# Performance work log

Measured on AMD Instinct MI355X. Metric: run time of the kernel, lower is better.

Reference implementation:

```python
import jax, jax.numpy as jnp
import numpy as np

MERGE_R = 2048


def setup_inputs() -> dict:
    key = jax.random.key(0)
    k1, k2 = jax.random.split(key, 2)
    B, N, C = 4, 8192, 512
    x = jax.random.normal(k1, (B, N, C), jnp.float32)
    W = jax.random.normal(k2, (C // 4, C), jnp.float32) * 0.02  # Linear(dim, dim//4)
    b = jnp.zeros((C // 4,), jnp.float32)
    return {"x": x, "W": W, "b": b}


def reference(x, W, b):
    B, N, C = x.shape
    r = min(MERGE_R, N // 2)

    # metric projection; matching is done under no_grad in the original
    metric = jax.lax.stop_gradient(x @ W.T + b)
    metric = metric / jnp.linalg.norm(metric, axis=-1, keepdims=True)

    a = metric[:, 0::2]   # [B, N/2, C/4] evens
    bt = metric[:, 1::2]  # [B, N/2, C/4] odds
    scores = jnp.einsum('bad,bcd->bac', a, bt)  # [B, N/2, N/2]
    values = scores.max(axis=-1)                # [B, N/2] best score per even token
    node_indices = scores.argmax(axis=-1)       # [B, N/2] best odd partner per even
    _, top_b_indices = jax.lax.top_k(values, r) # [B, r]

    bidx = jnp.arange(B)[:, None]
    global_b = top_b_indices * 2 + 1                                  # [B, r] odd positions removed
    matched_a = jnp.take_along_axis(node_indices, top_b_indices, 1)   # [B, r]
    global_a = matched_a * 2                                          # [B, r] even positions merged into

    # boolean keep-mask: exactly r False per row (topk indices are distinct)
    mask = jnp.ones((B, N), bool).at[bidx, global_b].set(False)

    b_feat = jnp.take_along_axis(x, global_b[:, :, None], axis=1)     # [B, r, C]
    x_out = x.at[bidx, global_a].add(b_feat)                          # scatter-add merge
    counts = jnp.ones((B, N, 1), x.dtype).at[bidx, global_a].add(1.0)
    x_out = x_out / counts

    # compact kept rows: stable argsort of ~mask keeps original order of True entries
    kept = jnp.argsort(~mask, axis=1)[:, : N - r]                     # [B, N-r]
    x_final = jnp.take_along_axis(x_out, kept[:, :, None], axis=1)    # [B, N-r, C]

    # ownership / unmerge map
    new_idx = jnp.cumsum(mask.astype(jnp.int32), axis=1) - 1          # [B, N]
    ownership = jnp.where(mask, new_idx, 0)
    target_a_new = jnp.take_along_axis(new_idx, global_a, axis=1)
    ownership = ownership.at[bidx, global_b].set(target_a_new)
    return x_final, ownership
```

## Files before the change

### kernel.cpp

```cpp
#include <hip/hip_runtime.h>
#include <cstdint>
#include <cstddef>

#define BQ    4
#define NTOK  8192
#define CDIM  512
#define MDIM  128
#define NA    4096
#define RSEL  2048
#define NKEEP (NTOK - RSEL)
#define RESCUE_CAP 2048
#define GAP_DELTA 2e-4f
#define WIN_TAU   2e-4f
#define CSPL  8

typedef float f32x4 __attribute__((ext_vector_type(4)));
typedef short short8 __attribute__((ext_vector_type(8)));

static __device__ __forceinline__ unsigned short bf16rne(float f) {
  unsigned u = __float_as_uint(f);
  return (unsigned short)((u + 0x7FFFu + ((u >> 16) & 1)) >> 16);
}

__device__ __forceinline__ unsigned long long rank_select_4096(
    const unsigned long long* keysL, unsigned* histL,
    unsigned long long* candL, unsigned* scanL, unsigned* shw ,
    int rank, int t) {
  unsigned long long pval = 0ull, pmask = 0ull;
  int curRank = rank;
  for (int lvl = 0; lvl < 3; ++lvl) {
    const int shift = 52 - lvl * 12;
#pragma unroll
    for (int i = 0; i < 4; ++i) histL[t + i * 1024] = 0;
    __syncthreads();
#pragma unroll
    for (int i = 0; i < 4; ++i) {
      unsigned long long k = keysL[t + i * 1024];
      if ((k & pmask) == pval)
        atomicAdd(&histL[(unsigned)((k >> shift) & 0xFFFull)], 1u);
    }
    __syncthreads();
    unsigned s = histL[4 * t] + histL[4 * t + 1] + histL[4 * t + 2] + histL[4 * t + 3];
    scanL[t] = s;
    __syncthreads();
    for (int off = 1; off < 1024; off <<= 1) {
      unsigned v = (t >= off) ? scanL[t - off] : 0;
      __syncthreads();
      scanL[t] += v;
      __syncthreads();
    }
    const unsigned incl = scanL[t], excl = incl - s;
    if ((int)excl <= curRank && curRank < (int)incl) {
      int r = curRank - (int)excl;
      unsigned b = 4 * t;
#pragma unroll
      for (int q = 0; q < 4; ++q) {
        unsigned c = histL[4 * t + q];
        if (r < (int)c) { b = 4 * t + q; break; }
        r -= (int)c;
      }
      shw[0] = b; shw[1] = (unsigned)r; shw[3] = histL[b];
    }
    __syncthreads();
    const unsigned bucket = shw[0];
    curRank = (int)shw[1];
    const unsigned cntB = shw[3];
    pval |= ((unsigned long long)bucket) << shift;
    pmask |= 0xFFFull << shift;
    if (cntB <= 1024u) break;
  }
  if (t == 0) shw[2] = 0;
  __syncthreads();
#pragma unroll
  for (int i = 0; i < 4; ++i) {
    unsigned long long k = keysL[t + i * 1024];
    if ((k & pmask) == pval) {
      unsigned pos = atomicAdd(&shw[2], 1u);
      if (pos < 1024u) candL[pos] = k;
    }
  }
  __syncthreads();
  const int c1 = (int)shw[2];
  int P = 64;
  while (P < c1) P <<= 1;
  for (int p = t; p < P; p += 1024)
    if (p >= c1) candL[p] = ~0ull;
  __syncthreads();
  for (int k2 = 2; k2 <= P; k2 <<= 1)
    for (int j = k2 >> 1; j > 0; j >>= 1) {
      for (int p = t; p < P; p += 1024) {
        int q = p ^ j;
        if (q > p) {
          bool up = ((p & k2) == 0);
          unsigned long long a = candL[p], c = candL[q];
          if ((a > c) == up) { candL[p] = c; candL[q] = a; }
        }
      }
      __syncthreads();
    }
  return candL[curRank];
}

__global__ __launch_bounds__(128) void k_metric(const float* __restrict__ X,
                                                const float* __restrict__ W,
                                                const float* __restrict__ bias,
                                                float* __restrict__ ma,
                                                float* __restrict__ mb,
                                                unsigned short* __restrict__ maH,
                                                unsigned short* __restrict__ maM,
                                                unsigned short* __restrict__ mbH,
                                                unsigned short* __restrict__ mbM) {
  __shared__ float ldsA[2][64 * 32];
  __shared__ float ldsB[2][128 * 32];
  __shared__ float snorm[64 * 16];
  __shared__ float sinv[64];
  const int t = threadIdx.x;
  const int tok0 = blockIdx.x * 64;
  const int r8 = t & 7, cg = t >> 3;

  float acc[8][8];
#pragma unroll
  for (int i = 0; i < 8; ++i)
#pragma unroll
    for (int j = 0; j < 8; ++j) acc[i][j] = 0.f;

  const char* aSrc[4];
  const char* bSrc[8];
#pragma unroll
  for (int i = 0; i < 4; ++i) {
    int s = i * 128 + t, row = s >> 3, gr = s & 7;
    aSrc[i] = (const char*)(X + (size_t)(tok0 + row) * CDIM) + ((gr ^ (row & 7)) << 4);
  }
#pragma unroll
  for (int i = 0; i < 8; ++i) {
    int s = i * 128 + t, row = s >> 3, gr = s & 7;
    bSrc[i] = (const char*)(W + (size_t)row * CDIM) + ((gr ^ ((row >> 3) & 7)) << 4);
  }

  auto stage = [&](int bufn, int kc) {
    const size_t off = (size_t)kc << 7;
    char* da = (char*)&ldsA[bufn][0] + t * 16;
    char* db = (char*)&ldsB[bufn][0] + t * 16;
#pragma unroll
    for (int i = 0; i < 4; ++i)
      __builtin_amdgcn_global_load_lds(
          (const __attribute__((address_space(1))) void*)(aSrc[i] + off),
          (__attribute__((address_space(3))) void*)(da + i * 2048), 16, 0, 0);
#pragma unroll
    for (int i = 0; i < 8; ++i)
      __builtin_amdgcn_global_load_lds(
          (const __attribute__((address_space(1))) void*)(bSrc[i] + off),
          (__attribute__((address_space(3))) void*)(db + i * 2048), 16, 0, 0);
  };

  auto compute = [&](int bufn) {
#pragma unroll
    for (int kq = 0; kq < 8; ++kq) {
      const int gA = (kq ^ r8) << 2;
      const int gB = (kq ^ (cg & 7)) << 2;
      float4 av[8], bv[8];
#pragma unroll
      for (int i = 0; i < 8; ++i)
        av[i] = *(const float4*)&ldsA[bufn][(r8 + (i << 3)) * 32 + gA];
#pragma unroll
      for (int j = 0; j < 8; ++j)
        bv[j] = *(const float4*)&ldsB[bufn][((cg << 3) + j) * 32 + gB];
#pragma unroll
      for (int i = 0; i < 8; ++i)
#pragma unroll
        for (int j = 0; j < 8; ++j) {
          acc[i][j] = fmaf(av[i].x, bv[j].x, acc[i][j]);
          acc[i][j] = fmaf(av[i].y, bv[j].y, acc[i][j]);
          acc[i][j] = fmaf(av[i].z, bv[j].z, acc[i][j]);
          acc[i][j] = fmaf(av[i].w, bv[j].w, acc[i][j]);
        }
    }
  };

  stage(0, 0);
  __syncthreads();
  for (int kc = 0; kc < 16; ++kc) {
    if (kc + 1 < 16) stage((kc + 1) & 1, kc + 1);
    compute(kc & 1);
    __syncthreads();
  }

  float bb[8];
#pragma unroll
  for (int j = 0; j < 8; ++j) bb[j] = bias[(cg << 3) + j];
#pragma unroll
  for (int i = 0; i < 8; ++i) {
    float s = 0.f;
#pragma unroll
    for (int j = 0; j < 8; ++j) {
      acc[i][j] += bb[j];
      s = fmaf(acc[i][j], acc[i][j], s);
    }
    snorm[(r8 + (i << 3)) * 16 + cg] = s;
  }
  __syncthreads();
  if (t < 64) {
    float s = 0.f;
    for (int q = 0; q < 16; ++q) s += snorm[t * 16 + q];
    sinv[t] = 1.0f / sqrtf(s);
  }
  __syncthreads();
#pragma unroll
  for (int i = 0; i < 8; ++i) {
    int r = r8 + (i << 3);
    int tokg = tok0 + r;
    float inv = sinv[r];
    int bq = tokg >> 13, pos = tokg & (NTOK - 1);
    size_t eidx = ((size_t)bq * NA + (pos >> 1)) * MDIM + (cg << 3);
    float vv[8];
#pragma unroll
    for (int j = 0; j < 8; ++j) vv[j] = acc[i][j] * inv;
    float* dst = ((pos & 1) ? mb : ma) + eidx;
    *(float4*)dst = make_float4(vv[0], vv[1], vv[2], vv[3]);
    *(float4*)(dst + 4) = make_float4(vv[4], vv[5], vv[6], vv[7]);
    unsigned hB[8], mB[8];
#pragma unroll
    for (int j = 0; j < 8; ++j) {
      hB[j] = bf16rne(vv[j]);
      mB[j] = bf16rne(vv[j] - __uint_as_float(hB[j] << 16));
    }
    uint4 hw, mw;
    hw.x = hB[0] | (hB[1] << 16); hw.y = hB[2] | (hB[3] << 16);
    hw.z = hB[4] | (hB[5] << 16); hw.w = hB[6] | (hB[7] << 16);
    mw.x = mB[0] | (mB[1] << 16); mw.y = mB[2] | (mB[3] << 16);
    mw.z = mB[4] | (mB[5] << 16); mw.w = mB[6] | (mB[7] << 16);
    *(uint4*)(((pos & 1) ? mbH : maH) + eidx) = hw;
    *(uint4*)(((pos & 1) ? mbM : maM) + eidx) = mw;
  }
}

__global__ __launch_bounds__(256, 4) void k_scores_mfma(
    const unsigned short* __restrict__ maH, const unsigned short* __restrict__ maM,
    const unsigned short* __restrict__ mbH, const unsigned short* __restrict__ mbM,
    float* __restrict__ pv1, int* __restrict__ pi1, float* __restrict__ pv2) {
  __shared__ short8 lds8[2][2][32][16];
  const int t = threadIdx.x;
  const int bid = blockIdx.x;
  const int bq = bid >> 9, rem = bid & 511, at = rem >> 3, cs = rem & 7;
  const int a0 = at * 64;
  const int l = t & 63, w = t >> 6;
  const int l15 = l & 15, l4 = l >> 4, l7 = l & 7;

  short8 aH[4], aM[4];
#pragma unroll
  for (int kc = 0; kc < 4; ++kc) {
    size_t aidx = ((size_t)bq * NA + a0 + w * 16 + l15) * MDIM + kc * 32 + l4 * 8;
    aH[kc] = *(const short8*)(maH + aidx);
    aM[kc] = *(const short8*)(maM + aidx);
  }

  const unsigned short* bplane = (w >> 1) ? mbM : mbH;
  const char* sp0; const char* sp1; const char* sp2; const char* sp3;
  {
    const int clb = (w & 1) * 16 + l4;
    const size_t rowb = (size_t)bq * NA + cs * 512;
    sp0 = (const char*)bplane + ((rowb + clb +  0) << 8) + ((l15 ^ ((clb +  0) & 7)) << 4);
    sp1 = (const char*)bplane + ((rowb + clb +  4) << 8) + ((l15 ^ ((clb +  4) & 7)) << 4);
    sp2 = (const char*)bplane + ((rowb + clb +  8) << 8) + ((l15 ^ ((clb +  8) & 7)) << 4);
    sp3 = (const char*)bplane + ((rowb + clb + 12) << 8) + ((l15 ^ ((clb + 12) & 7)) << 4);
  }

  float bv1[4], bv2[4];
  int bi1[4];
#pragma unroll
  for (int s = 0; s < 4; ++s) { bv1[s] = -1e30f; bv2[s] = -1e30f; bi1[s] = 0x7FFFFFFF; }

  auto stage = [&](int bufn) {
    char* dst = (char*)&lds8[bufn][0][0][0] + w * 4096 + l * 16;
    __builtin_amdgcn_global_load_lds((const __attribute__((address_space(1))) void*)sp0,
        (__attribute__((address_space(3))) void*)(dst + 0),    16, 0, 0);
    __builtin_amdgcn_global_load_lds((const __attribute__((address_space(1))) void*)sp1,
        (__attribute__((address_space(3))) void*)(dst + 1024), 16, 0, 0);
    __builtin_amdgcn_global_load_lds((const __attribute__((address_space(1))) void*)sp2,
        (__attribute__((address_space(3))) void*)(dst + 2048), 16, 0, 0);
    __builtin_amdgcn_global_load_lds((const __attribute__((address_space(1))) void*)sp3,
        (__attribute__((address_space(3))) void*)(dst + 3072), 16, 0, 0);
    sp0 += 8192; sp1 += 8192; sp2 += 8192; sp3 += 8192;
  };

  auto compute = [&](int bufn, int cbase) {
    f32x4 acc1[2], acc2[2];
    acc1[0] = 0.f; acc1[1] = 0.f; acc2[0] = 0.f; acc2[1] = 0.f;
#pragma unroll
    for (int kc = 0; kc < 4; ++kc) {
      const int gg = (kc * 4 + l4) ^ l7;
#pragma unroll
      for (int cf = 0; cf < 2; ++cf) {
        short8 bh = lds8[bufn][0][cf * 16 + l15][gg];
        short8 bm = lds8[bufn][1][cf * 16 + l15][gg];
        acc1[cf] = __builtin_amdgcn_mfma_f32_16x16x32_bf16(aH[kc], bh, acc1[cf], 0, 0, 0);
        acc2[cf] = __builtin_amdgcn_mfma_f32_16x16x32_bf16(aH[kc], bm, acc2[cf], 0, 0, 0);
        acc2[cf] = __builtin_amdgcn_mfma_f32_16x16x32_bf16(aM[kc], bh, acc2[cf], 0, 0, 0);
      }
    }
#pragma unroll
    for (int cf = 0; cf < 2; ++cf) {
      const int cg = cbase + cf * 16 + l15;
      f32x4 v4 = acc1[cf] + acc2[cf];
#pragma unroll
      for (int r2 = 0; r2 < 4; ++r2) {
        float v = v4[r2];
        if (v > bv1[r2]) { bv2[r2] = bv1[r2]; bv1[r2] = v; bi1[r2] = cg; }
        else if (v > bv2[r2]) bv2[r2] = v;
      }
    }
  };

  stage(0);
  __syncthreads();
  const int cb0 = cs * 512;
  for (int chp = 0; chp < 8; ++chp) {
    const int ch = chp * 2;
    if (ch + 1 < 16) stage(1);
    compute(0, cb0 + ch * 32);
    __syncthreads();
    if (ch + 2 < 16) stage(0);
    compute(1, cb0 + ch * 32 + 32);
    __syncthreads();
  }

#pragma unroll
  for (int s = 0; s < 4; ++s) {
    float v1 = bv1[s], v2 = bv2[s];
    int i1 = bi1[s];
#pragma unroll
    for (int m = 1; m < 16; m <<= 1) {
      float V1 = __shfl_xor(v1, m);
      int I1 = __shfl_xor(i1, m);
      float V2 = __shfl_xor(v2, m);
      bool take = (V1 > v1) || (V1 == v1 && I1 < i1);
      float lose = take ? v1 : V1;
      if (take) { v1 = V1; i1 = I1; }
      v2 = fmaxf(fmaxf(v2, V2), lose);
    }
    if (l15 == s) {
      int row = a0 + w * 16 + l4 * 4 + s;
      size_t off = ((size_t)(bq * CSPL + cs)) * NA + row;
      pv1[off] = v1; pi1[off] = i1; pv2[off] = v2;
    }
  }
}

__global__ __launch_bounds__(1024) void k_mergemark(
    const float* __restrict__ pv1, const int* __restrict__ pi1,
    const float* __restrict__ pv2,
    float* __restrict__ valA, int* __restrict__ nodeA,
    int* __restrict__ rescueCnt, int* __restrict__ rescueIdx,
    int* __restrict__ cnt, int* __restrict__ head,
    unsigned long long* __restrict__ rescueKey) {
  __shared__ unsigned long long keys[NA];
  __shared__ unsigned hist[NA];
  __shared__ unsigned long long cand[1024];
  __shared__ unsigned scan1[1024];
  __shared__ unsigned shw[4];
  const int b = blockIdx.x, t = threadIdx.x;
  if (t == 0) rescueCnt[b] = 0;
  float gval[4], ggap[4];
#pragma unroll
  for (int k4 = 0; k4 < 4; ++k4) {
    const int p = t + k4 * 1024;
    const size_t i = (size_t)b * NA + p;
    float v1 = -1e30f, v2 = -1e30f;
    int i1 = 0x7FFFFFFF;
#pragma unroll
    for (int cspl = 0; cspl < CSPL; ++cspl) {
      size_t o = ((size_t)(b * CSPL + cspl)) * NA + p;
      float V1 = pv1[o], V2 = pv2[o];
      int I1 = pi1[o];
      bool take = (V1 > v1) || (V1 == v1 && I1 < i1);
      float lose = take ? v1 : V1;
      if (take) { v1 = V1; i1 = I1; }
      v2 = fmaxf(fmaxf(v2, V2), lose);
    }
    valA[i] = v1; nodeA[i] = i1;
    cnt[i] = 0; head[i] = -1; rescueKey[i] = 0ull;
    gval[k4] = v1; ggap[k4] = v1 - v2;
    unsigned u = __float_as_uint(v1);
    unsigned mono = u ^ ((u >> 31) ? 0xFFFFFFFFu : 0x80000000u);
    keys[p] = ((unsigned long long)(~mono) << 32) | (unsigned)p;
  }
  __syncthreads();

  const unsigned long long thr =
      rank_select_4096(keys, hist, cand, scan1, shw, RSEL - 1, t);
  unsigned monoT = ~(unsigned)(thr >> 32);
  unsigned uT = (monoT >> 31) ? (monoT ^ 0x80000000u) : ~monoT;
  const float vb = __uint_as_float(uT);

#pragma unroll
  for (int k4 = 0; k4 < 4; ++k4) {
    const int p = t + k4 * 1024;
    if (ggap[k4] < GAP_DELTA || fabsf(gval[k4] - vb) <= WIN_TAU) {
      int slot = atomicAdd(&rescueCnt[b], 1);
      if (slot < RESCUE_CAP) rescueIdx[b * RESCUE_CAP + slot] = p;
    }
  }
}

__global__ __launch_bounds__(256) void k_rescue(const float* __restrict__ ma,
                                                const float* __restrict__ mb,
                                                const int* __restrict__ rescueIdx,
                                                const int* __restrict__ rescueCnt,
                                                unsigned long long* __restrict__ key) {
  const int bq = blockIdx.x >> 8;
  const int wid = blockIdx.x & 255;
  const int cnt = min(rescueCnt[bq], RESCUE_CAP);
  const int npair = cnt * 16;
  const int t = threadIdx.x;
  __shared__ float sA[128];
  __shared__ float wv[4];
  __shared__ int   wi[4];
  for (int pair = wid; pair < npair; pair += 256) {
    const int slot = pair >> 4, chunk = pair & 15;
    const int row = rescueIdx[bq * RESCUE_CAP + slot];
    __syncthreads();
    if (t < 128) sA[t] = ma[((size_t)bq * NA + row) * MDIM + t];
    __syncthreads();
    const int c = chunk * 256 + t;
    const float* bp = mb + ((size_t)bq * NA + c) * MDIM;
    float d0 = 0.f, d1 = 0.f, d2 = 0.f, d3 = 0.f;
#pragma unroll
    for (int j = 0; j < 8; ++j) {
      float4 b0 = *(const float4*)(bp + j * 16 + 0);
      float4 b1 = *(const float4*)(bp + j * 16 + 4);
      float4 b2 = *(const float4*)(bp + j * 16 + 8);
      float4 b3 = *(const float4*)(bp + j * 16 + 12);
      const float4 a0 = *(const float4*)&sA[j * 16 + 0];
      const float4 a1 = *(const float4*)&sA[j * 16 + 4];
      const float4 a2 = *(const float4*)&sA[j * 16 + 8];
      const float4 a3 = *(const float4*)&sA[j * 16 + 12];
      d0 = fmaf(a0.x, b0.x, d0); d0 = fmaf(a0.y, b0.y, d0);
      d0 = fmaf(a0.z, b0.z, d0); d0 = fmaf(a0.w, b0.w, d0);
      d1 = fmaf(a1.x, b1.x, d1); d1 = fmaf(a1.y, b1.y, d1);
      d1 = fmaf(a1.z, b1.z, d1); d1 = fmaf(a1.w, b1.w, d1);
      d2 = fmaf(a2.x, b2.x, d2); d2 = fmaf(a2.y, b2.y, d2);
      d2 = fmaf(a2.z, b2.z, d2); d2 = fmaf(a2.w, b2.w, d2);
      d3 = fmaf(a3.x, b3.x, d3); d3 = fmaf(a3.y, b3.y, d3);
      d3 = fmaf(a3.z, b3.z, d3); d3 = fmaf(a3.w, b3.w, d3);
    }
    float d = (d0 + d1) + (d2 + d3);
    int ci = c;
#pragma unroll
    for (int m = 1; m < 64; m <<= 1) {
      float V = __shfl_xor(d, m);
      int C = __shfl_xor(ci, m);
      if (V > d || (V == d && C < ci)) { d = V; ci = C; }
    }
    if ((t & 63) == 0) { wv[t >> 6] = d; wi[t >> 6] = ci; }
    __syncthreads();
    if (t == 0) {
      for (int w2 = 1; w2 < 4; ++w2)
        if (wv[w2] > d || (wv[w2] == d && wi[w2] < ci)) { d = wv[w2]; ci = wi[w2]; }
      unsigned u = __float_as_uint(d);
      unsigned mono = u ^ ((u >> 31) ? 0xFFFFFFFFu : 0x80000000u);
      unsigned long long k = ((unsigned long long)mono << 32)
                           | (unsigned)(0xFFFFFFFFu - (unsigned)ci);
      atomicMax(&key[(size_t)bq * NA + row], k);
    }
  }
}

__global__ __launch_bounds__(1024) void k_select(
    const unsigned long long* __restrict__ rescueKey,
    const float* __restrict__ valA, const int* __restrict__ nodeA,
    int* __restrict__ sel, int* __restrict__ cnt, int* __restrict__ head,
    int* __restrict__ nxt, int* __restrict__ newidx,
    float* __restrict__ own) {
  __shared__ unsigned long long keys[NA];
  __shared__ int nodeL[NA];
  __shared__ unsigned char selL[NA];
  __shared__ int ni[NTOK];
  __shared__ unsigned tot[1024];
  __shared__ unsigned hist[NA];
  __shared__ unsigned long long cand[1024];
  __shared__ unsigned shw[4];
  const int b = blockIdx.x, t = threadIdx.x;

#pragma unroll
  for (int k4 = 0; k4 < 4; ++k4) {
    const int p = t + k4 * 1024;
    const size_t i = (size_t)b * NA + p;
    unsigned long long rk = rescueKey[i];
    float v; int nd;
    if (rk) {
      unsigned mono = (unsigned)(rk >> 32);
      unsigned u = (mono & 0x80000000u) ? (mono ^ 0x80000000u) : ~mono;
      v = __uint_as_float(u);
      nd = (int)(0xFFFFFFFFu - (unsigned)(rk & 0xFFFFFFFFull));
    } else {
      v = valA[i];
      nd = nodeA[i];
    }
    nodeL[p] = nd;
    unsigned u = __float_as_uint(v);
    unsigned mono = u ^ ((u >> 31) ? 0xFFFFFFFFu : 0x80000000u);
    keys[p] = ((unsigned long long)(~mono) << 32) | (unsigned)p;
  }
  __syncthreads();

  const unsigned long long thr =
      rank_select_4096(keys, hist, cand, tot, shw, RSEL - 1, t);

#pragma unroll
  for (int k4 = 0; k4 < 4; ++k4) {
    const int p = t + k4 * 1024;
    selL[p] = (keys[p] <= thr) ? 1 : 0;
  }
  __syncthreads();

#pragma unroll
  for (int k4 = 0; k4 < 4; ++k4) {
    const int p = t + k4 * 1024;
    const size_t i = (size_t)b * NA + p;
    int s = selL[p];
    sel[i] = s;
    if (s) {
      int dst = nodeL[p];
      atomicAdd(&cnt[(size_t)b * NA + dst], 1);
      nxt[i] = atomicExch(&head[(size_t)b * NA + dst], p);
    }
  }

  const int base = t * 8;
  int kept[8], run = 0;
#pragma unroll
  for (int e = 0; e < 8; ++e) {
    int idx = base + e;
    int kp = ((idx & 1) == 0) ? 1 : (selL[idx >> 1] ? 0 : 1);
    kept[e] = kp;
    run += kp;
  }
  tot[t] = (unsigned)run;
  __syncthreads();
  for (int off = 1; off < 1024; off <<= 1) {
    unsigned v = (t >= off) ? tot[t - off] : 0;
    __syncthreads();
    tot[t] += v;
    __syncthreads();
  }
  int cum = (int)tot[t] - run;
#pragma unroll
  for (int e = 0; e < 8; ++e) {
    cum += kept[e];
    ni[base + e] = cum - 1;
  }
  __syncthreads();
#pragma unroll
  for (int e = 0; e < 8; ++e) {
    int idx = base + e;
    int ow = kept[e] ? ni[idx] : ni[2 * nodeL[idx >> 1]];
    newidx[(size_t)b * NTOK + idx] = ni[idx];
    own[(size_t)b * NTOK + idx] = (float)ow;
  }
}

__global__ __launch_bounds__(256) void k_assemble(const float* __restrict__ X,
                                                  const int* __restrict__ sel,
                                                  const int* __restrict__ newidx,
                                                  const int* __restrict__ cnt,
                                                  const int* __restrict__ head,
                                                  const int* __restrict__ nxt,
                                                  float* __restrict__ out) {
  const int token = blockIdx.x * 2 + (threadIdx.x >> 7);
  const int bq = token >> 13, tp = token & (NTOK - 1);
  const int t = threadIdx.x & 127;
  if ((tp & 1) && sel[(size_t)bq * NA + (tp >> 1)]) return;
  float4 v = *(const float4*)(X + (size_t)token * CDIM + t * 4);
  if (!(tp & 1)) {
    size_t slot = (size_t)bq * NA + (tp >> 1);
    int c = cnt[slot];
    if (c > 0) {
      int kk = head[slot];
      while (kk >= 0) {
        float4 s = *(const float4*)(X + ((size_t)bq * NTOK + 2 * kk + 1) * CDIM + t * 4);
        v.x += s.x; v.y += s.y; v.z += s.z; v.w += s.w;
        kk = nxt[(size_t)bq * NA + kk];
      }
      float inv = 1.0f / (float)(1 + c);
      v.x *= inv; v.y *= inv; v.z *= inv; v.w *= inv;
    }
  }
  int dst = newidx[(size_t)bq * NTOK + tp];
  *(float4*)(out + ((size_t)bq * NKEEP + dst) * CDIM + t * 4) = v;
}

extern "C" void kernel_launch(void* const* d_in, const int* in_sizes, int n_in,
                              void* d_out, int out_size, void* d_ws, size_t ws_size,
                              hipStream_t stream) {
  const float* X    = (const float*)d_in[0];
  const float* W    = (const float*)d_in[1];
  const float* bias = (const float*)d_in[2];
  float* out = (float*)d_out;
  char* ws = (char*)d_ws;

  size_t o = 0;
  float* ma   = (float*)(ws + o); o += (size_t)BQ * NA * MDIM * 4;
  float* mb   = (float*)(ws + o); o += (size_t)BQ * NA * MDIM * 4;
  unsigned short* maH = (unsigned short*)(ws + o); o += (size_t)BQ * NA * MDIM * 2;
  unsigned short* maM = (unsigned short*)(ws + o); o += (size_t)BQ * NA * MDIM * 2;
  unsigned short* mbH = (unsigned short*)(ws + o); o += (size_t)BQ * NA * MDIM * 2;
  unsigned short* mbM = (unsigned short*)(ws + o); o += (size_t)BQ * NA * MDIM * 2;
  float* pv1  = (float*)(ws + o); o += (size_t)BQ * CSPL * NA * 4;
  int*   pi1  = (int*)(ws + o);   o += (size_t)BQ * CSPL * NA * 4;
  float* pv2  = (float*)(ws + o); o += (size_t)BQ * CSPL * NA * 4;
  float* valA = (float*)(ws + o); o += (size_t)BQ * NA * 4;
  int*   nodeA= (int*)(ws + o);   o += (size_t)BQ * NA * 4;
  int*   sel  = (int*)(ws + o);   o += (size_t)BQ * NA * 4;
  int*   cnt  = (int*)(ws + o);   o += (size_t)BQ * NA * 4;
  int*   head = (int*)(ws + o);   o += (size_t)BQ * NA * 4;
  int*   nxt  = (int*)(ws + o);   o += (size_t)BQ * NA * 4;
  int*   newidx = (int*)(ws + o); o += (size_t)BQ * NTOK * 4;
  int*   rescueCnt = (int*)(ws + o); o += 256;
  int*   rescueIdx = (int*)(ws + o); o += (size_t)BQ * RESCUE_CAP * 4;
  unsigned long long* rescueKey = (unsigned long long*)(ws + o); o += (size_t)BQ * NA * 8;
  (void)in_sizes; (void)n_in; (void)out_size; (void)ws_size;

  k_metric<<<512, 128, 0, stream>>>(X, W, bias, ma, mb, maH, maM, mbH, mbM);
  k_scores_mfma<<<BQ * 64 * CSPL, 256, 0, stream>>>(maH, maM, mbH, mbM, pv1, pi1, pv2);
  k_mergemark<<<BQ, 1024, 0, stream>>>(pv1, pi1, pv2, valA, nodeA,
                                       rescueCnt, rescueIdx, cnt, head, rescueKey);
  k_rescue<<<BQ * 256, 256, 0, stream>>>(ma, mb, rescueIdx, rescueCnt, rescueKey);
  k_select<<<BQ, 1024, 0, stream>>>(rescueKey, valA, nodeA, sel, cnt, head, nxt,
                                    newidx, out + (size_t)BQ * NKEEP * CDIM);
  k_assemble<<<BQ * NTOK / 2, 256, 0, stream>>>(X, sel, newidx, cnt, head, nxt, out);
}
```

Before: 274.1 us.

## Read W directly from global in metric GEMM and double block threads

The metric projection kernel drops LDS staging of the weight matrix and has each thread load its 8 W rows straight from global memory (expected to hit L2/L1), while doubling the block to 256 threads with a 4x8 accumulator tile per thread. This removes half the LDS traffic and staging instructions and raises occupancy through fewer registers per thread. In exchange, every thread issues scattered global float4 loads of W per k-step, which adds memory latency and may not coalesce well.

After: 283.6 us. 3.5% more time.

```diff
diff --git a/kernel.cpp b/kernel.cpp
--- a/kernel.cpp
+++ b/kernel.cpp
@@ -101,7 +101,7 @@
   return candL[curRank];
 }
 
-__global__ __launch_bounds__(128) void k_metric(const float* __restrict__ X,
+__global__ __launch_bounds__(256) void k_metric(const float* __restrict__ X,
                                                 const float* __restrict__ W,
                                                 const float* __restrict__ bias,
                                                 float* __restrict__ ma,
@@ -111,62 +111,51 @@
                                                 unsigned short* __restrict__ mbH,
                                                 unsigned short* __restrict__ mbM) {
   __shared__ float ldsA[2][64 * 32];
-  __shared__ float ldsB[2][128 * 32];
   __shared__ float snorm[64 * 16];
   __shared__ float sinv[64];
   const int t = threadIdx.x;
   const int tok0 = blockIdx.x * 64;
-  const int r8 = t & 7, cg = t >> 3;
-
-  float acc[8][8];
-#pragma unroll
-  for (int i = 0; i < 8; ++i)
+  const int r16 = t & 15, cg = t >> 4;
+
+  float acc[4][8];
+#pragma unroll
+  for (int i = 0; i < 4; ++i)
 #pragma unroll
     for (int j = 0; j < 8; ++j) acc[i][j] = 0.f;
 
-  const char* aSrc[4];
-  const char* bSrc[8];
-#pragma unroll
-  for (int i = 0; i < 4; ++i) {
-    int s = i * 128 + t, row = s >> 3, gr = s & 7;
-    aSrc[i] = (const char*)(X + (size_t)(tok0 + row) * CDIM) + ((gr ^ (row & 7)) << 4);
-  }
-#pragma unroll
-  for (int i = 0; i < 8; ++i) {
-    int s = i * 128 + t, row = s >> 3, gr = s & 7;
-    bSrc[i] = (const char*)(W + (size_t)row * CDIM) + ((gr ^ ((row >> 3) & 7)) << 4);
+  const char* aSrc[2];
+#pragma unroll
+  for (int i = 0; i < 2; ++i) {
+    int s = i * 256 + t, row = s >> 3, g = s & 7;
+    aSrc[i] = (const char*)(X + (size_t)(tok0 + row) * CDIM) + ((g ^ (row & 7)) << 4);
   }
 
   auto stage = [&](int bufn, int kc) {
     const size_t off = (size_t)kc << 7;
     char* da = (char*)&ldsA[bufn][0] + t * 16;
-    char* db = (char*)&ldsB[bufn][0] + t * 16;
-#pragma unroll
-    for (int i = 0; i < 4; ++i)
+#pragma unroll
+    for (int i = 0; i < 2; ++i)
       __builtin_amdgcn_global_load_lds(
           (const __attribute__((address_space(1))) void*)(aSrc[i] + off),
-          (__attribute__((address_space(3))) void*)(da + i * 2048), 16, 0, 0);
-#pragma unroll
-    for (int i = 0; i < 8; ++i)
-      __builtin_amdgcn_global_load_lds(
-          (const __attribute__((address_space(1))) void*)(bSrc[i] + off),
-          (__attribute__((address_space(3))) void*)(db + i * 2048), 16, 0, 0);
+          (__attribute__((address_space(3))) void*)(da + i * 4096), 16, 0, 0);
   };
 
-  auto compute = [&](int bufn) {
+  const float* wBase = W + (size_t)(cg << 3) * CDIM;
+
+  auto compute = [&](int bufn, int kc) {
 #pragma unroll
     for (int kq = 0; kq < 8; ++kq) {
-      const int gA = (kq ^ r8) << 2;
-      const int gB = (kq ^ (cg & 7)) << 2;
-      float4 av[8], bv[8];
-#pragma unroll
-      for (int i = 0; i < 8; ++i)
-        av[i] = *(const float4*)&ldsA[bufn][(r8 + (i << 3)) * 32 + gA];
+      const int gA = (kq ^ (r16 & 7)) << 2;
+      float4 av[4];
+#pragma unroll
+      for (int i = 0; i < 4; ++i)
+        av[i] = *(const float4*)&ldsA[bufn][(r16 + (i << 4)) * 32 + gA];
+      float4 bv[8];
 #pragma unroll
       for (int j = 0; j < 8; ++j)
-        bv[j] = *(const float4*)&ldsB[bufn][((cg << 3) + j) * 32 + gB];
-#pragma unroll
-      for (int i = 0; i < 8; ++i)
+        bv[j] = *(const float4*)(wBase + (size_t)j * CDIM + kc * 32 + kq * 4);
+#pragma unroll
+      for (int i = 0; i < 4; ++i)
 #pragma unroll
         for (int j = 0; j < 8; ++j) {
           acc[i][j] = fmaf(av[i].x, bv[j].x, acc[i][j]);
@@ -181,7 +170,7 @@
   __syncthreads();
   for (int kc = 0; kc < 16; ++kc) {
     if (kc + 1 < 16) stage((kc + 1) & 1, kc + 1);
-    compute(kc & 1);
+    compute(kc & 1, kc);
     __syncthreads();
   }
 
@@ -189,14 +178,14 @@
 #pragma unroll
   for (int j = 0; j < 8; ++j) bb[j] = bias[(cg << 3) + j];
 #pragma unroll
-  for (int i = 0; i < 8; ++i) {
+  for (int i = 0; i < 4; ++i) {
     float s = 0.f;
 #pragma unroll
     for (int j = 0; j < 8; ++j) {
       acc[i][j] += bb[j];
       s = fmaf(acc[i][j], acc[i][j], s);
     }
-    snorm[(r8 + (i << 3)) * 16 + cg] = s;
+    snorm[(r16 + (i << 4)) * 16 + cg] = s;
   }
   __syncthreads();
   if (t < 64) {
@@ -206,8 +195,8 @@
   }
   __syncthreads();
 #pragma unroll
-  for (int i = 0; i < 8; ++i) {
-    int r = r8 + (i << 3);
+  for (int i = 0; i < 4; ++i) {
+    int r = r16 + (i << 4);
     int tokg = tok0 + r;
     float inv = sinv[r];
     int bq = tokg >> 13, pos = tokg & (NTOK - 1);
@@ -620,7 +609,7 @@
   unsigned long long* rescueKey = (unsigned long long*)(ws + o); o += (size_t)BQ * NA * 8;
   (void)in_sizes; (void)n_in; (void)out_size; (void)ws_size;
 
-  k_metric<<<512, 128, 0, stream>>>(X, W, bias, ma, mb, maH, maM, mbH, mbM);
+  k_metric<<<512, 256, 0, stream>>>(X, W, bias, ma, mb, maH, maM, mbH, mbM);
   k_scores_mfma<<<BQ * 64 * CSPL, 256, 0, stream>>>(maH, maM, mbH, mbM, pv1, pi1, pv2);
   k_mergemark<<<BQ, 1024, 0, stream>>>(pv1, pi1, pv2, valA, nodeA,
                                        rescueCnt, rescueIdx, cnt, head, rescueKey);
```

## Retile scores MFMA kernel to 32 rows per wave and 16-way column split

Applied to the files above, without the earlier changes.

Reshapes the score kernel's tile so each wave keeps two 16-row A fragments in registers and reuses every LDS-loaded B fragment across both. Blocks now cover 128 A rows, and the column split doubles to 16. This halves LDS B reads per MFMA and halves total global B traffic. In exchange it uses more registers (launch bound lowered to 3 blocks per CU) and doubles the per-split partial max buffers that the merge kernel must reduce.

New measurement: 316.4 us. 15.4% more time.

```diff
diff --git a/kernel.cpp b/kernel.cpp
--- a/kernel.cpp
+++ b/kernel.cpp
@@ -12,7 +12,7 @@
 #define RESCUE_CAP 2048
 #define GAP_DELTA 2e-4f
 #define WIN_TAU   2e-4f
-#define CSPL  8
+#define CSPL  16
 
 typedef float f32x4 __attribute__((ext_vector_type(4)));
 typedef short short8 __attribute__((ext_vector_type(8)));
@@ -234,98 +234,95 @@
   }
 }
 
-__global__ __launch_bounds__(256, 4) void k_scores_mfma(
+__global__ __launch_bounds__(256, 3) void k_scores_mfma(
     const unsigned short* __restrict__ maH, const unsigned short* __restrict__ maM,
     const unsigned short* __restrict__ mbH, const unsigned short* __restrict__ mbM,
     float* __restrict__ pv1, int* __restrict__ pi1, float* __restrict__ pv2) {
-  __shared__ short8 lds8[2][2][32][16];
+  __shared__ short8 lds8[2][2][16][16];
   const int t = threadIdx.x;
   const int bid = blockIdx.x;
-  const int bq = bid >> 9, rem = bid & 511, at = rem >> 3, cs = rem & 7;
-  const int a0 = at * 64;
+  const int bq = bid >> 9, rem = bid & 511, at = rem >> 4, cs = rem & 15;
+  const int a0 = at * 128;
   const int l = t & 63, w = t >> 6;
-  const int l15 = l & 15, l4 = l >> 4, l7 = l & 7;
-
-  short8 aH[4], aM[4];
-#pragma unroll
-  for (int kc = 0; kc < 4; ++kc) {
-    size_t aidx = ((size_t)bq * NA + a0 + w * 16 + l15) * MDIM + kc * 32 + l4 * 8;
-    aH[kc] = *(const short8*)(maH + aidx);
-    aM[kc] = *(const short8*)(maM + aidx);
-  }
-
-  const unsigned short* bplane = (w >> 1) ? mbM : mbH;
-  const char* sp0; const char* sp1; const char* sp2; const char* sp3;
-  {
-    const int clb = (w & 1) * 16 + l4;
-    const size_t rowb = (size_t)bq * NA + cs * 512;
-    sp0 = (const char*)bplane + ((rowb + clb +  0) << 8) + ((l15 ^ ((clb +  0) & 7)) << 4);
-    sp1 = (const char*)bplane + ((rowb + clb +  4) << 8) + ((l15 ^ ((clb +  4) & 7)) << 4);
-    sp2 = (const char*)bplane + ((rowb + clb +  8) << 8) + ((l15 ^ ((clb +  8) & 7)) << 4);
-    sp3 = (const char*)bplane + ((rowb + clb + 12) << 8) + ((l15 ^ ((clb + 12) & 7)) << 4);
-  }
-
-  float bv1[4], bv2[4];
-  int bi1[4];
-#pragma unroll
-  for (int s = 0; s < 4; ++s) { bv1[s] = -1e30f; bv2[s] = -1e30f; bi1[s] = 0x7FFFFFFF; }
+  const int l15 = l & 15, l4 = l >> 4;
+
+  short8 aH[2][4], aM[2][4];
+#pragma unroll
+  for (int rf = 0; rf < 2; ++rf)
+#pragma unroll
+    for (int kc = 0; kc < 4; ++kc) {
+      size_t aidx = ((size_t)bq * NA + a0 + w * 32 + rf * 16 + l15) * MDIM
+                    + kc * 32 + l4 * 8;
+      aH[rf][kc] = *(const short8*)(maH + aidx);
+      aM[rf][kc] = *(const short8*)(maM + aidx);
+    }
+
+  const int scl = t >> 4, sg = t & 15;
+  const size_t srow = ((size_t)bq * NA + cs * 256 + scl) << 8;
+  const size_t soff = srow + (size_t)((sg ^ (scl & 7)) << 4);
+  const char* spH = (const char*)mbH + soff;
+  const char* spM = (const char*)mbM + soff;
 
   auto stage = [&](int bufn) {
-    char* dst = (char*)&lds8[bufn][0][0][0] + w * 4096 + l * 16;
-    __builtin_amdgcn_global_load_lds((const __attribute__((address_space(1))) void*)sp0,
-        (__attribute__((address_space(3))) void*)(dst + 0),    16, 0, 0);
-    __builtin_amdgcn_global_load_lds((const __attribute__((address_space(1))) void*)sp1,
-        (__attribute__((address_space(3))) void*)(dst + 1024), 16, 0, 0);
-    __builtin_amdgcn_global_load_lds((const __attribute__((address_space(1))) void*)sp2,
-        (__attribute__((address_space(3))) void*)(dst + 2048), 16, 0, 0);
-    __builtin_amdgcn_global_load_lds((const __attribute__((address_space(1))) void*)sp3,
-        (__attribute__((address_space(3))) void*)(dst + 3072), 16, 0, 0);
-    sp0 += 8192; sp1 += 8192; sp2 += 8192; sp3 += 8192;
+    char* dst = (char*)&lds8[bufn][0][0][0] + t * 16;
+    __builtin_amdgcn_global_load_lds(
+        (const __attribute__((address_space(1))) void*)spH,
+        (__attribute__((address_space(3))) void*)dst, 16, 0, 0);
+    __builtin_amdgcn_global_load_lds(
+        (const __attribute__((address_space(1))) void*)spM,
+        (__attribute__((address_space(3))) void*)(dst + 4096), 16, 0, 0);
+    spH += 4096; spM += 4096;
   };
+
+  float bv1[8], bv2[8];
+  int bi1[8];
+#pragma unroll
+  for (int s = 0; s < 8; ++s) { bv1[s] = -1e30f; bv2[s] = -1e30f; bi1[s] = 0x7FFFFFFF; }
 
   auto compute = [&](int bufn, int cbase) {
     f32x4 acc1[2], acc2[2];
     acc1[0] = 0.f; acc1[1] = 0.f; acc2[0] = 0.f; acc2[1] = 0.f;
 #pragma unroll
     for (int kc = 0; kc < 4; ++kc) {
-      const int gg = (kc * 4 + l4) ^ l7;
-#pragma unroll
-      for (int cf = 0; cf < 2; ++cf) {
-        short8 bh = lds8[bufn][0][cf * 16 + l15][gg];
-        short8 bm = lds8[bufn][1][cf * 16 + l15][gg];
-        acc1[cf] = __builtin_amdgcn_mfma_f32_16x16x32_bf16(aH[kc], bh, acc1[cf], 0, 0, 0);
-        acc2[cf] = __builtin_amdgcn_mfma_f32_16x16x32_bf16(aH[kc], bm, acc2[cf], 0, 0, 0);
-        acc2[cf] = __builtin_amdgcn_mfma_f32_16x16x32_bf16(aM[kc], bh, acc2[cf], 0, 0, 0);
+      const int gg = (kc * 4 + l4) ^ (l15 & 7);
+      short8 bh = lds8[bufn][0][l15][gg];
+      short8 bm = lds8[bufn][1][l15][gg];
+#pragma unroll
+      for (int rf = 0; rf < 2; ++rf) {
+        acc1[rf] = __builtin_amdgcn_mfma_f32_16x16x32_bf16(aH[rf][kc], bh, acc1[rf], 0, 0, 0);
+        acc2[rf] = __builtin_amdgcn_mfma_f32_16x16x32_bf16(aH[rf][kc], bm, acc2[rf], 0, 0, 0);
+        acc2[rf] = __builtin_amdgcn_mfma_f32_16x16x32_bf16(aM[rf][kc], bh, acc2[rf], 0, 0, 0);
       }
     }
-#pragma unroll
-    for (int cf = 0; cf < 2; ++cf) {
-      const int cg = cbase + cf * 16 + l15;
-      f32x4 v4 = acc1[cf] + acc2[cf];
+    const int cg = cbase + l15;
+#pragma unroll
+    for (int rf = 0; rf < 2; ++rf) {
+      f32x4 v4 = acc1[rf] + acc2[rf];
 #pragma unroll
       for (int r2 = 0; r2 < 4; ++r2) {
         float v = v4[r2];
-        if (v > bv1[r2]) { bv2[r2] = bv1[r2]; bv1[r2] = v; bi1[r2] = cg; }
-        else if (v > bv2[r2]) bv2[r2] = v;
+        int s = rf * 4 + r2;
+        if (v > bv1[s]) { bv2[s] = bv1[s]; bv1[s] = v; bi1[s] = cg; }
+        else if (v > bv2[s]) bv2[s] = v;
       }
     }
   };
 
   stage(0);
   __syncthreads();
-  const int cb0 = cs * 512;
+  const int cb0 = cs * 256;
   for (int chp = 0; chp < 8; ++chp) {
     const int ch = chp * 2;
     if (ch + 1 < 16) stage(1);
-    compute(0, cb0 + ch * 32);
+    compute(0, cb0 + ch * 16);
     __syncthreads();
     if (ch + 2 < 16) stage(0);
-    compute(1, cb0 + ch * 32 + 32);
-    __syncthreads();
-  }
-
-#pragma unroll
-  for (int s = 0; s < 4; ++s) {
+    compute(1, cb0 + ch * 16 + 16);
+    __syncthreads();
+  }
+
+#pragma unroll
+  for (int s = 0; s < 8; ++s) {
     float v1 = bv1[s], v2 = bv2[s];
     int i1 = bi1[s];
 #pragma unroll
@@ -339,7 +336,7 @@
       v2 = fmaxf(fmaxf(v2, V2), lose);
     }
     if (l15 == s) {
-      int row = a0 + w * 16 + l4 * 4 + s;
+      int row = a0 + w * 32 + (s >> 2) * 16 + (l4 << 2) + (s & 3);
       size_t off = ((size_t)(bq * CSPL + cs)) * NA + row;
       pv1[off] = v1; pi1[off] = i1; pv2[off] = v2;
     }
@@ -621,7 +618,7 @@
   (void)in_sizes; (void)n_in; (void)out_size; (void)ws_size;
 
   k_metric<<<512, 128, 0, stream>>>(X, W, bias, ma, mb, maH, maM, mbH, mbM);
-  k_scores_mfma<<<BQ * 64 * CSPL, 256, 0, stream>>>(maH, maM, mbH, mbM, pv1, pi1, pv2);
+  k_scores_mfma<<<BQ * 32 * CSPL, 256, 0, stream>>>(maH, maM, mbH, mbM, pv1, pi1, pv2);
   k_mergemark<<<BQ, 1024, 0, stream>>>(pv1, pi1, pv2, valA, nodeA,
                                        rescueCnt, rescueIdx, cnt, head, rescueKey);
   k_rescue<<<BQ * 256, 256, 0, stream>>>(ma, mb, rescueIdx, rescueCnt, rescueKey);
```
